# Performance work log

Hardware: AMD Instinct MI355X
Metric: run time of the kernel (lower is better)

## Reference

```python
import jax, jax.numpy as jnp
import numpy as np

B = 1; NUM_Q = 200; PREFIX = 5; GH = 40; GW = 40; P = GH * GW
N = NUM_Q + PREFIX + P  # 1805, token layout [queries][prefix][patches]
D = 1024; NH = 16; DH = D // NH; NB = 4; NC = 151
NEG = -1e9  # additive stand-in for the boolean SDPA mask


def _ln(x, g, b):
    m = x.mean(-1, keepdims=True)
    v = ((x - m) ** 2).mean(-1, keepdims=True)
    return (x - m) * jax.lax.rsqrt(v + 1e-6) * g + b


def setup_inputs() -> dict:
    key = jax.random.key(0)
    ks = iter(jax.random.split(key, 16))
    rn = lambda shape, s=0.02: jax.random.normal(next(ks), shape, jnp.float32) * s
    return {
        'x_tokens': jax.random.normal(next(ks), (B, PREFIX + P, D), jnp.float32),
        'q_weight': rn((NUM_Q, D), 1.0),
        'norm_g': jnp.ones((D,)), 'norm_b': jnp.zeros((D,)),
        'class_W': rn((D, NC)), 'class_b': jnp.zeros((NC,)),
        'mask_W1': rn((D, D)), 'mask_b1': jnp.zeros((D,)),
        'mask_W2': rn((D, D)), 'mask_b2': jnp.zeros((D,)),
        'mask_W3': rn((D, D)), 'mask_b3': jnp.zeros((D,)),
        'ln1_g': jnp.ones((NB, D)), 'ln1_b': jnp.zeros((NB, D)),
        'ln2_g': jnp.ones((NB, D)), 'ln2_b': jnp.zeros((NB, D)),
        'qkv_W': rn((NB, D, 3 * D)), 'qkv_b': jnp.zeros((NB, 3 * D)),
        'proj_W': rn((NB, D, D)), 'proj_b': jnp.zeros((NB, D)),
        'ls1': 0.1 * jnp.ones((NB, D)), 'ls2': 0.1 * jnp.ones((NB, D)),
        'fc1_W': rn((NB, D, 4 * D)), 'fc1_b': jnp.zeros((NB, 4 * D)),
        'fc2_W': rn((NB, 4 * D, D)), 'fc2_b': jnp.zeros((NB, D)),
    }


def _forward(x_tokens, q_weight, norm_g, norm_b, class_W, class_b,
             mask_W1, mask_b1, mask_W2, mask_b2, mask_W3, mask_b3,
             ln1_g, ln1_b, ln2_g, ln2_b, qkv_W, qkv_b, proj_W, proj_b,
             ls1, ls2, fc1_W, fc1_b, fc2_W, fc2_b):
    scale = 1.0 / np.sqrt(DH)
    gelu = lambda t: jax.nn.gelu(t, approximate=False)  # torch nn.GELU (erf)

    def predict(nx):
        # _predict: class head + 3-layer mask MLP + einsum('bqc,bchw->bqhw') decode
        q = nx[:, :NUM_Q]
        patch = nx[:, NUM_Q + PREFIX:]  # [B, P, D] == patch_tokens_map flattened
        f = gelu(q @ mask_W1 + mask_b1)
        f = gelu(f @ mask_W2 + mask_b2)
        f = f @ mask_W3 + mask_b3
        mask_logits = jnp.einsum('bqc,bpc->bqp', f, patch).reshape(B, NUM_Q, GH, GW)
        class_logits = q @ class_W + class_b
        return mask_logits, class_logits

    def attn_bias(mask_logits):
        # _attn_mask: bilinear interp to grid, >0 threshold, rows=queries, cols=patches.
        # attn_mask_probs == 1 so _disable_attn_mask is a no-op.
        interp = jax.image.resize(mask_logits, (B, NUM_Q, GH, GW), 'bilinear')
        keep = interp.reshape(B, NUM_Q, P) > 0
        qrows = jnp.where(keep, 0.0, NEG)  # [B, q, P]
        return jnp.zeros((B, N, N), jnp.float32).at[:, :NUM_Q, NUM_Q + PREFIX:].set(qrows)

    def block(x, i, bias):
        h = _ln(x, ln1_g[i], ln1_b[i])
        qkv = (h @ qkv_W[i] + qkv_b[i]).reshape(B, N, 3, NH, DH)
        qh = qkv[:, :, 0].transpose(0, 2, 1, 3)  # [B, H, N, DH]
        kh = qkv[:, :, 1].transpose(0, 2, 1, 3)
        vh = qkv[:, :, 2].transpose(0, 2, 1, 3)
        scores = jnp.einsum('bhnd,bhmd->bhnm', qh, kh) * scale + bias[:, None]
        a = jax.nn.softmax(scores, axis=-1)
        o = jnp.einsum('bhnm,bhmd->bhnd', a, vh).transpose(0, 2, 1, 3).reshape(B, N, D)
        x = x + ls1[i] * (o @ proj_W[i] + proj_b[i])
        h2 = _ln(x, ln2_g[i], ln2_b[i])
        x = x + ls2[i] * (gelu(h2 @ fc1_W[i] + fc1_b[i]) @ fc2_W[i] + fc2_b[i])
        return x

    x = jnp.concatenate([jnp.broadcast_to(q_weight, (B, NUM_Q, D)), x_tokens], axis=1)
    masks, classes = [], []
    for i in range(NB):  # fixed 4 late blocks
        nx = _ln(x, norm_g, norm_b)
        m, c = predict(nx)
        masks.append(m); classes.append(c)
        x = block(x, i, attn_bias(m))
    nx = _ln(x, norm_g, norm_b)
    m, c = predict(nx)
    masks.append(m); classes.append(c)
    return jnp.stack(masks), jnp.stack(classes)


def reference(x_tokens, q_weight, norm_g, norm_b, class_W, class_b,
              mask_W1, mask_b1, mask_W2, mask_b2, mask_W3, mask_b3,
              ln1_g, ln1_b, ln2_g, ln2_b, qkv_W, qkv_b, proj_W, proj_b,
              ls1, ls2, fc1_W, fc1_b, fc2_W, fc2_b):
    return _forward(x_tokens, q_weight, norm_g, norm_b, class_W, class_b,
                    mask_W1, mask_b1, mask_W2, mask_b2, mask_W3, mask_b3,
                    ln1_g, ln1_b, ln2_g, ln2_b, qkv_W, qkv_b, proj_W, proj_b,
                    ls1, ls2, fc1_W, fc1_b, fc2_W, fc2_b)
```

## Files before the change

kernel.cpp:

```cpp
#include <hip/hip_runtime.h>
#include <hip/hip_bf16.h>

#define NQ 200
#define PFX 5
#define NPATCH 1600
#define NT 1805
#define DM 1024
#define NHEAD 16
#define DHEAD 64
#define NBLK 4
#define NCLS 151
#define NKT 29
#define NWRD 57

typedef short s16x8 __attribute__((ext_vector_type(8)));
typedef float f32x4 __attribute__((ext_vector_type(4)));

__device__ __forceinline__ float gelu_f(float x) {
  return 0.5f * x * (1.0f + erff(x * 0.7071067811865476f));
}
__device__ __forceinline__ short f2bf(float x) {
  __hip_bfloat16 h = __float2bfloat16(x);
  return *reinterpret_cast<short*>(&h);
}
__device__ __forceinline__ float bf2f(short s) {
  __hip_bfloat16 h;
  *reinterpret_cast<short*>(&h) = s;
  return __bfloat162float(h);
}
__device__ __forceinline__ void glds16(const void* g, void* l) {
  __builtin_amdgcn_global_load_lds(
      (const __attribute__((address_space(1))) void*)g,
      (__attribute__((address_space(3))) void*)l, 16, 0, 0);
}

__global__ __launch_bounds__(256) void concat_kernel(const float* __restrict__ qw,
    const float* __restrict__ xt, float* __restrict__ x) {
  int idx = blockIdx.x * 256 + threadIdx.x;
  if (idx >= NT * DM) return;
  int n = idx >> 10;
  x[idx] = (n < NQ) ? qw[idx] : xt[idx - NQ * DM];
}

__global__ __launch_bounds__(256) void cvtT_kernel(const float* __restrict__ W,
    short* __restrict__ Th, short* __restrict__ Tl, int K, int N) {
  __shared__ float t[32][33];
  const int n0 = blockIdx.x * 32, k0 = blockIdx.y * 32;
  const int tx = threadIdx.x & 31, ty = threadIdx.x >> 5;
#pragma unroll
  for (int i = 0; i < 32; i += 8)
    t[ty + i][tx] = W[(size_t)(k0 + ty + i) * N + n0 + tx];
  __syncthreads();
#pragma unroll
  for (int i = 0; i < 32; i += 8) {
    int n = n0 + ty + i, k = k0 + tx;
    float xv = t[tx][ty + i];
    short hh = f2bf(xv);
    Th[(size_t)n * K + k] = hh;
    Tl[(size_t)n * K + k] = f2bf(xv - bf2f(hh));
  }
}

__global__ __launch_bounds__(256) void ln_kernel(const float* __restrict__ in,
    const float* __restrict__ g, const float* __restrict__ b,
    short* __restrict__ oh, short* __restrict__ ol) {
  const int row = blockIdx.x;
  const int tid = threadIdx.x;
  const float* x = in + (size_t)row * DM;
  float v[4];
#pragma unroll
  for (int i = 0; i < 4; ++i) v[i] = x[tid + (i << 8)];
  float s = v[0] + v[1] + v[2] + v[3];
  __shared__ float red[4];
  __shared__ float red2[4];
#pragma unroll
  for (int off = 32; off; off >>= 1) s += __shfl_down(s, off, 64);
  if ((tid & 63) == 0) red[tid >> 6] = s;
  __syncthreads();
  float mean = (red[0] + red[1] + red[2] + red[3]) * (1.0f / DM);
  float sq = 0.f;
#pragma unroll
  for (int i = 0; i < 4; ++i) { float d = v[i] - mean; sq += d * d; }
#pragma unroll
  for (int off = 32; off; off >>= 1) sq += __shfl_down(sq, off, 64);
  if ((tid & 63) == 0) red2[tid >> 6] = sq;
  __syncthreads();
  float var = (red2[0] + red2[1] + red2[2] + red2[3]) * (1.0f / DM);
  float inv = 1.0f / sqrtf(var + 1e-6f);
#pragma unroll
  for (int i = 0; i < 4; ++i) {
    int d = tid + (i << 8);
    float y = (v[i] - mean) * inv * g[d] + b[d];
    short hh = f2bf(y);
    oh[(size_t)row * DM + d] = hh;
    ol[(size_t)row * DM + d] = f2bf(y - bf2f(hh));
  }
}

template <int BM64, int BSRC, int ALO, int ACT, int OMODE, int KS>
__global__ __launch_bounds__(256) void mgemm_kernel(
    const short* __restrict__ Ah, const short* __restrict__ Al,
    const float* __restrict__ Wf,
    const short* __restrict__ Bh, const short* __restrict__ Bl,
    const float* __restrict__ bias, const float* __restrict__ lsv,
    float* __restrict__ Cf, short* __restrict__ Ch, short* __restrict__ Cl,
    int M, int N, int K) {
  constexpr int BM = BM64 ? 64 : 128;
  constexpr int AT = BM64 ? 2 : 4;
  constexpr int AISS = BM64 ? 1 : 2;
  __shared__ __align__(16) short sAh[2 * BM * 32];
  __shared__ __align__(16) short sAl[ALO ? 2 * BM * 32 : 8];
  __shared__ __align__(16) short sBh[2 * 128 * 32], sBl[2 * 128 * 32];
  const int tid = threadIdx.x;
  const int lane = tid & 63;
  const int w = tid >> 6;
  const int bm = blockIdx.y * BM;
  const int bn = blockIdx.x << 7;
  const int z = (KS > 1) ? blockIdx.z : 0;
  const int KL = K / KS;
  const int kbase = z * KL;

  f32x4 acc[AT][4];
  {
    f32x4 zf = {0.f, 0.f, 0.f, 0.f};
#pragma unroll
    for (int mi = 0; mi < AT; ++mi)
#pragma unroll
      for (int ni = 0; ni < 4; ++ni) acc[mi][ni] = zf;
  }

  auto issueA = [&](int buf, int k0) {
#pragma unroll
    for (int i = 0; i < AISS; ++i) {
      int br = (BM64 ? (w << 4) : (w << 5) + (i << 4));
      int r = br + (lane >> 2);
      int cg = (lane & 3) ^ ((r >> 1) & 3);
      size_t go = (size_t)min(bm + r, M - 1) * K + kbase + k0 + (cg << 3);
      glds16(Ah + go, &sAh[(buf * BM + br) * 32]);
      if (ALO) glds16(Al + go, &sAl[(buf * BM + br) * 32]);
    }
  };
  auto issueB1 = [&](int buf, int k0) {
#pragma unroll
    for (int i = 0; i < 2; ++i) {
      int br = (w << 5) + (i << 4);
      int r = br + (lane >> 2);
      int cg = (lane & 3) ^ ((r >> 1) & 3);
      size_t go = (size_t)min(bn + r, N - 1) * K + kbase + k0 + (cg << 3);
      glds16(Bh + go, &sBh[(buf * 128 + br) * 32]);
      glds16(Bl + go, &sBl[(buf * 128 + br) * 32]);
    }
  };
  float wv[2][8];
  auto loadB0 = [&](int k0) {
#pragma unroll
    for (int p = 0; p < 2; ++p) {
      int n = tid & 127;
      int c8 = (tid >> 7) + (p << 1);
      const float* Wp = Wf + (size_t)(kbase + k0 + (c8 << 3)) * N + min(bn + n, N - 1);
#pragma unroll
      for (int j = 0; j < 8; ++j) wv[p][j] = Wp[(size_t)j * N];
    }
  };
  auto writeB0 = [&](int buf) {
#pragma unroll
    for (int p = 0; p < 2; ++p) {
      int n = tid & 127;
      int c8 = (tid >> 7) + (p << 1);
      int cp = c8 ^ ((n >> 1) & 3);
      union { uint4 u; short e[8]; } H, L;
#pragma unroll
      for (int j = 0; j < 8; ++j) {
        short hh = f2bf(wv[p][j]);
        H.e[j] = hh;
        L.e[j] = f2bf(wv[p][j] - bf2f(hh));
      }
      int off = (buf * 128 + n) * 32 + (cp << 3);
      *(uint4*)&sBh[off] = H.u;
      *(uint4*)&sBl[off] = L.u;
    }
  };

  issueA(0, 0);
  if (BSRC == 1) issueB1(0, 0);
  else { loadB0(0); writeB0(0); }
  __syncthreads();

  const int nt = KL >> 5;
  int cur = 0;
  const int ar = lane & 15;
  const int kc = lane >> 4;
  const int wmr = BM64 ? ((w >> 1) << 5) : ((w >> 1) << 6);
  const int wnr = (w & 1) << 6;

  for (int t = 0; t < nt; ++t) {
    const bool more = (t + 1 < nt);
    if (more) {
      int k0n = (t + 1) << 5;
      issueA(cur ^ 1, k0n);
      if (BSRC == 1) issueB1(cur ^ 1, k0n);
      else loadB0(k0n);
    }
    s16x8 fah[AT], fal[AT], fbh[4], fbl[4];
#pragma unroll
    for (int t2 = 0; t2 < AT; ++t2) {
      int r = wmr + (t2 << 4) + ar;
      int off = (cur * BM + r) * 32 + ((kc ^ ((r >> 1) & 3)) << 3);
      fah[t2] = *(const s16x8*)&sAh[off];
      if (ALO) fal[t2] = *(const s16x8*)&sAl[off];
    }
#pragma unroll
    for (int t2 = 0; t2 < 4; ++t2) {
      int r = wnr + (t2 << 4) + ar;
      int off = (cur * 128 + r) * 32 + ((kc ^ ((r >> 1) & 3)) << 3);
      fbh[t2] = *(const s16x8*)&sBh[off];
      fbl[t2] = *(const s16x8*)&sBl[off];
    }
#pragma unroll
    for (int mi = 0; mi < AT; ++mi)
#pragma unroll
      for (int ni = 0; ni < 4; ++ni) {
        acc[mi][ni] = __builtin_amdgcn_mfma_f32_16x16x32_bf16(fah[mi], fbh[ni], acc[mi][ni], 0, 0, 0);
        acc[mi][ni] = __builtin_amdgcn_mfma_f32_16x16x32_bf16(fah[mi], fbl[ni], acc[mi][ni], 0, 0, 0);
        if (ALO)
          acc[mi][ni] = __builtin_amdgcn_mfma_f32_16x16x32_bf16(fal[mi], fbh[ni], acc[mi][ni], 0, 0, 0);
      }
    if (more) {
      if (BSRC == 0) writeB0(cur ^ 1);
      __syncthreads();
      cur ^= 1;
    }
  }

  const int erow = bm + wmr + ((lane >> 4) << 2);
  const int ecol = bn + wnr + (lane & 15);
  float bv[4], lv[4];
#pragma unroll
  for (int ni = 0; ni < 4; ++ni) {
    int col = ecol + ni * 16;
    float b0 = (bias != nullptr && col < N) ? bias[col] : 0.f;
    bv[ni] = (KS > 1 && z != 0) ? 0.f : b0;
    lv[ni] = (OMODE == 5 && col < N) ? lsv[col] : 0.f;
  }
#pragma unroll
  for (int mi = 0; mi < AT; ++mi) {
#pragma unroll
    for (int rr = 0; rr < 4; ++rr) {
      int row = erow + mi * 16 + rr;
      if (row >= M) continue;
#pragma unroll
      for (int ni = 0; ni < 4; ++ni) {
        int col = ecol + ni * 16;
        if (col >= N) continue;
        float v = acc[mi][ni][rr] + bv[ni];
        size_t o = (size_t)row * N + col;
        if (OMODE == 0) {
          if (ACT == 1) v = gelu_f(v);
          short hh = f2bf(v);
          Ch[o] = hh;
          Cl[o] = f2bf(v - bf2f(hh));
        } else if (OMODE == 1) {
          if (ACT == 1) v = gelu_f(v);
          Cf[o] = v;
        } else if (OMODE == 2) {
          atomicAdd(&Cf[o], v);
        } else if (OMODE == 3) {
          Cf[(size_t)z * M * N + o] = v;
        } else if (OMODE == 4) {
          if (ACT == 1) v = gelu_f(v);
          Ch[o] = f2bf(v);
        } else if (OMODE == 5) {
          atomicAdd(&Cf[o], lv[ni] * v);
        } else {
          short hh = f2bf(v);
          Ch[o] = hh;
          if (col < 1024) Cl[o] = f2bf(v - bf2f(hh));
        }
      }
    }
  }
}

template <int ACT, int WSPLIT>
__global__ __launch_bounds__(256) void redsplit_kernel(const float* __restrict__ pb,
    float* __restrict__ outf, short* __restrict__ oh, short* __restrict__ ol,
    int KSr, int MN) {
  int idx = blockIdx.x * 256 + threadIdx.x;
  if (idx >= MN) return;
  float s = 0.f;
  for (int zz = 0; zz < KSr; ++zz) s += pb[(size_t)zz * MN + idx];
  if (ACT == 1) s = gelu_f(s);
  if (WSPLIT) {
    short hh = f2bf(s);
    oh[idx] = hh;
    ol[idx] = f2bf(s - bf2f(hh));
  } else {
    outf[idx] = s;
  }
}

__global__ __launch_bounds__(256) void maskpack_kernel(const float* __restrict__ mlog,
    unsigned* __restrict__ bits) {
  int idx = blockIdx.x * 256 + threadIdx.x;
  if (idx >= NQ * NWRD) return;
  int q = idx / NWRD, w = idx - q * NWRD;
  unsigned word = 0u;
  int c0 = w * 32;
#pragma unroll
  for (int b = 0; b < 32; ++b) {
    int c = c0 + b;
    unsigned keep;
    if (c < NQ + PFX) keep = 1u;
    else if (c < NT) keep = (mlog[(size_t)q * NPATCH + (c - NQ - PFX)] > 0.f) ? 1u : 0u;
    else keep = 0u;
    word |= keep << b;
  }
  bits[idx] = word;
}

__global__ __launch_bounds__(256, 2) void fattn_kernel(
    const short* __restrict__ qh, const short* __restrict__ ql,
    const unsigned* __restrict__ bits, short* __restrict__ ao_h) {
  const int bid = blockIdx.x;
  const int h = bid & 15;
  const int q0 = (bid >> 4) * 64;
  const int tid = threadIdx.x;
  const int lane = tid & 63;
  const int w = tid >> 6;
  const int lg = lane >> 4;
  const int lc = lane & 15;

  __shared__ __align__(16) short Kh[2 * 64 * 64];
  __shared__ __align__(16) short Vt[2 * 64 * 64];
  __shared__ __align__(16) short Pp[4][16 * 64];
  __shared__ float fb[4][16];

  s16x8 qfh[2], qfl[2];
  {
    int gq = min(q0 + (w << 4) + lc, NT - 1);
    const size_t base = (size_t)gq * 3072 + h * 64;
#pragma unroll
    for (int ks = 0; ks < 2; ++ks) {
      qfh[ks] = *(const s16x8*)(qh + base + ks * 32 + (lg << 3));
      qfl[ks] = *(const s16x8*)(ql + base + ks * 32 + (lg << 3));
    }
  }

  const int krow = tid >> 3, kchk = tid & 7;
  const int vrow = tid >> 2, vchk = tid & 3;
  uint4 pkh[2], pvh[2];
  auto loadKV = [&](int kt) {
#pragma unroll
    for (int ii = 0; ii < 2; ++ii) {
      int gk = kt * 64 + krow + (ii << 5);
      if (gk < NT) {
        pkh[ii] = *(const uint4*)(qh + (size_t)gk * 3072 + 1024 + h * 64 + (kchk << 3));
      } else {
        pkh[ii] = make_uint4(0, 0, 0, 0);
      }
      int gv = kt * 64 + vrow;
      int vc = vchk + (ii << 2);
      if (gv < NT) {
        pvh[ii] = *(const uint4*)(qh + (size_t)gv * 3072 + 2048 + h * 64 + (vc << 3));
      } else {
        pvh[ii] = make_uint4(0, 0, 0, 0);
      }
    }
  };
  auto writeKV = [&](int buf) {
    const int bo = buf << 12;
#pragma unroll
    for (int ii = 0; ii < 2; ++ii) {
      int row = krow + (ii << 5);
      *(uint4*)&Kh[bo + (row << 6) + ((kchk ^ (row & 7)) << 3)] = pkh[ii];
      int vc = vchk + (ii << 2);
      const short* vs = (const short*)&pvh[ii];
#pragma unroll
      for (int jj = 0; jj < 8; ++jj) {
        int d = (vc << 3) + jj;
        Vt[bo + (d << 6) + (((vrow >> 3) ^ (d & 7)) << 3) + (vrow & 7)] = vs[jj];
      }
    }
  };

  float rm_r[4], rl_r[4];
#pragma unroll
  for (int r = 0; r < 4; ++r) { rm_r[r] = -3.0e38f; rl_r[r] = 0.f; }
  f32x4 o_acc[4];
  {
    f32x4 zf = {0.f, 0.f, 0.f, 0.f};
#pragma unroll
    for (int nd = 0; nd < 4; ++nd) o_acc[nd] = zf;
  }

  loadKV(0);
  writeKV(0);
  __syncthreads();
  loadKV(1);

  for (int kt = 0; kt < NKT; ++kt) {
    const int cb = (kt & 1) << 12;

    f32x4 sc[4];
    {
      f32x4 zf = {0.f, 0.f, 0.f, 0.f};
#pragma unroll
      for (int ni = 0; ni < 4; ++ni) sc[ni] = zf;
    }
    __builtin_amdgcn_s_setprio(1);
#pragma unroll
    for (int ni = 0; ni < 4; ++ni) {
#pragma unroll
      for (int ks = 0; ks < 2; ++ks) {
        int row = (ni << 4) + lc;
        int ch = ((ks << 2) + lg) ^ (row & 7);
        s16x8 kh = *(const s16x8*)&Kh[cb + (row << 6) + (ch << 3)];
        sc[ni] = __builtin_amdgcn_mfma_f32_16x16x32_bf16(qfh[ks], kh, sc[ni], 0, 0, 0);
        sc[ni] = __builtin_amdgcn_mfma_f32_16x16x32_bf16(qfl[ks], kh, sc[ni], 0, 0, 0);
      }
    }
    __builtin_amdgcn_s_setprio(0);

    unsigned wr0[4], wr1[4];
#pragma unroll
    for (int r = 0; r < 4; ++r) {
      int gq = q0 + (w << 4) + (lg << 2) + r;
      wr0[r] = 0xFFFFFFFFu; wr1[r] = 0xFFFFFFFFu;
      if (gq < NQ) {
        wr0[r] = bits[gq * NWRD + (kt << 1)];
        wr1[r] = ((kt << 1) + 1 < NWRD) ? bits[gq * NWRD + (kt << 1) + 1] : 0u;
      }
    }
    const int kvb = kt << 6;
#pragma unroll
    for (int ni = 0; ni < 4; ++ni) {
      int kv = kvb + (ni << 4) + lc;
      unsigned bitpos = ((ni & 1) << 4) + lc;
#pragma unroll
      for (int r = 0; r < 4; ++r) {
        float sv = sc[ni][r] * 0.125f;
        unsigned wd = (ni < 2) ? wr0[r] : wr1[r];
        if (!((wd >> bitpos) & 1u)) sv -= 1e9f;
        sc[ni][r] = (kv < NT) ? sv : -3.0e38f;
      }
    }

    float fr[4];
#pragma unroll
    for (int r = 0; r < 4; ++r) {
      float tm = fmaxf(fmaxf(sc[0][r], sc[1][r]), fmaxf(sc[2][r], sc[3][r]));
#pragma unroll
      for (int m2 = 1; m2 < 16; m2 <<= 1) tm = fmaxf(tm, __shfl_xor(tm, m2, 64));
      float mnew = fmaxf(rm_r[r], tm);
      float f = __expf(rm_r[r] - mnew);
      float ps = 0.f;
#pragma unroll
      for (int ni = 0; ni < 4; ++ni) {
        float e = __expf(sc[ni][r] - mnew);
        sc[ni][r] = e;
        ps += e;
      }
#pragma unroll
      for (int m2 = 1; m2 < 16; m2 <<= 1) ps += __shfl_xor(ps, m2, 64);
      rm_r[r] = mnew;
      rl_r[r] = rl_r[r] * f + ps;
      fr[r] = f;
    }

    short* P = Pp[w];
#pragma unroll
    for (int ni = 0; ni < 4; ++ni) {
#pragma unroll
      for (int r = 0; r < 4; ++r) {
        int qq = (lg << 2) + r;
        int col = (ni << 4) + lc;
        P[(qq << 6) + (((col >> 3) ^ (qq & 7)) << 3) + (col & 7)] = f2bf(sc[ni][r]);
      }
    }
    if (lc == 0) {
#pragma unroll
      for (int r = 0; r < 4; ++r) fb[w][(lg << 2) + r] = fr[r];
    }
    float fq = fb[w][lc];
#pragma unroll
    for (int nd = 0; nd < 4; ++nd)
#pragma unroll
      for (int r = 0; r < 4; ++r) o_acc[nd][r] *= fq;

    s16x8 pfrag[2];
#pragma unroll
    for (int ks = 0; ks < 2; ++ks)
      pfrag[ks] = *(const s16x8*)&P[(lc << 6) + ((((ks << 2) + lg) ^ (lc & 7)) << 3)];
    __builtin_amdgcn_s_setprio(1);
#pragma unroll
    for (int nd = 0; nd < 4; ++nd) {
      int row = (nd << 4) + lc;
#pragma unroll
      for (int ks = 0; ks < 2; ++ks) {
        s16x8 vh = *(const s16x8*)&Vt[cb + (row << 6) + ((((ks << 2) + lg) ^ (lc & 7)) << 3)];
        o_acc[nd] = __builtin_amdgcn_mfma_f32_16x16x32_bf16(vh, pfrag[ks], o_acc[nd], 0, 0, 0);
      }
    }
    __builtin_amdgcn_s_setprio(0);

    if (kt + 1 < NKT) {
      writeKV((kt + 1) & 1);
      if (kt + 2 < NKT) loadKV(kt + 2);
      __syncthreads();
    }
  }

  if (lc == 0) {
#pragma unroll
    for (int r = 0; r < 4; ++r) fb[w][(lg << 2) + r] = rl_r[r];
  }
  float inv = 1.0f / fb[w][lc];
  int gq = q0 + (w << 4) + lc;
  if (gq < NT) {
#pragma unroll
    for (int nd = 0; nd < 4; ++nd) {
      short hh[4];
#pragma unroll
      for (int r = 0; r < 4; ++r) hh[r] = f2bf(o_acc[nd][r] * inv);
      size_t o = (size_t)gq * DM + h * 64 + (nd << 4) + (lg << 2);
      *(short4*)(ao_h + o) = make_short4(hh[0], hh[1], hh[2], hh[3]);
    }
  }
}

extern "C" void kernel_launch(void* const* d_in, const int* in_sizes, int n_in,
                              void* d_out, int out_size, void* d_ws, size_t ws_size,
                              hipStream_t stream) {
  const float* x_tokens = (const float*)d_in[0];
  const float* q_weight = (const float*)d_in[1];
  const float* norm_g   = (const float*)d_in[2];
  const float* norm_b   = (const float*)d_in[3];
  const float* class_W  = (const float*)d_in[4];
  const float* class_b  = (const float*)d_in[5];
  const float* mask_W1  = (const float*)d_in[6];
  const float* mask_b1  = (const float*)d_in[7];
  const float* mask_W2  = (const float*)d_in[8];
  const float* mask_b2  = (const float*)d_in[9];
  const float* mask_W3  = (const float*)d_in[10];
  const float* mask_b3  = (const float*)d_in[11];
  const float* ln1_g    = (const float*)d_in[12];
  const float* ln1_b    = (const float*)d_in[13];
  const float* ln2_g    = (const float*)d_in[14];
  const float* ln2_b    = (const float*)d_in[15];
  const float* qkv_W    = (const float*)d_in[16];
  const float* qkv_b    = (const float*)d_in[17];
  const float* proj_W   = (const float*)d_in[18];
  const float* proj_b   = (const float*)d_in[19];
  const float* ls1      = (const float*)d_in[20];
  const float* ls2      = (const float*)d_in[21];
  const float* fc1_W    = (const float*)d_in[22];
  const float* fc1_b    = (const float*)d_in[23];
  const float* fc2_W    = (const float*)d_in[24];
  const float* fc2_b    = (const float*)d_in[25];

  float* out = (float*)d_out;

  char* p = (char*)d_ws;
  auto alloc = [&](size_t bytes) {
    char* r = p;
    p += (bytes + 255) & ~(size_t)255;
    return r;
  };
  float* x     = (float*)alloc((size_t)NT * DM * 4);
  short* lnb_h = (short*)alloc((size_t)NT * DM * 2);
  short* lnb_l = (short*)alloc((size_t)NT * DM * 2);
  char*  A1    = alloc((size_t)NT * 4 * DM * 4);
  char*  A2    = alloc((size_t)NT * 4 * DM * 2);
  unsigned* bias_bits = (unsigned*)alloc((size_t)NQ * NWRD * 4);

  short* qkvh  = (short*)A1;
  short* qkvl  = qkvh + (size_t)NT * 3 * DM;
  short* fTh   = (short*)A1;
  short* fTl   = fTh + (size_t)4 * DM * DM;
  short* f1_h = (short*)A1;
  short* f1_l = f1_h + (size_t)NQ * DM;
  short* f2_h = f1_l + (size_t)NQ * DM;
  short* f2_l = f2_h + (size_t)NQ * DM;
  short* f3_h = f2_l + (size_t)NQ * DM;
  short* f3_l = f3_h + (size_t)NQ * DM;
  float* pbuf = (float*)(A1 + ((size_t)4 << 20));
  short* qTh   = (short*)A2;
  short* qTl   = qTh + (size_t)3 * DM * DM;
  short* aoh   = (short*)A2;
  short* pTh   = (short*)(A2 + (size_t)NT * DM * 4);
  short* pTl   = pTh + (size_t)DM * DM;
  short* g1h   = (short*)A2;

  const int ELEM_GRID = (NT * DM + 255) / 256;
  auto g128 = [](int M, int Nc, int ks) { return dim3((Nc + 127) / 128, (M + 127) / 128, ks); };
  auto g64  = [](int M, int Nc, int ks) { return dim3((Nc + 127) / 128, (M + 63) / 64, ks); };
  auto rgrid = [](int n) { return dim3((n + 255) / 256); };
  auto cgrid = [](int K, int N) { return dim3(N / 32, K / 32); };

  concat_kernel<<<ELEM_GRID, 256, 0, stream>>>(q_weight, x_tokens, x);

  for (int i = 0; i <= NBLK; ++i) {
    ln_kernel<<<NT, 256, 0, stream>>>(x, norm_g, norm_b, lnb_h, lnb_l);
    float* mask_i = out + (size_t)i * NQ * NPATCH;
    float* cls_i  = out + (size_t)5 * NQ * NPATCH + (size_t)i * NQ * NCLS;
    mgemm_kernel<1, 0, 1, 0, 3, 8><<<g64(NQ, DM, 8), 256, 0, stream>>>(
        lnb_h, lnb_l, mask_W1, nullptr, nullptr, mask_b1, nullptr, pbuf, nullptr, nullptr, NQ, DM, DM);
    redsplit_kernel<1, 1><<<rgrid(NQ * DM), 256, 0, stream>>>(pbuf, nullptr, f1_h, f1_l, 8, NQ * DM);
    mgemm_kernel<1, 0, 1, 0, 3, 8><<<g64(NQ, DM, 8), 256, 0, stream>>>(
        f1_h, f1_l, mask_W2, nullptr, nullptr, mask_b2, nullptr, pbuf, nullptr, nullptr, NQ, DM, DM);
    redsplit_kernel<1, 1><<<rgrid(NQ * DM), 256, 0, stream>>>(pbuf, nullptr, f2_h, f2_l, 8, NQ * DM);
    mgemm_kernel<1, 0, 1, 0, 3, 8><<<g64(NQ, DM, 8), 256, 0, stream>>>(
        f2_h, f2_l, mask_W3, nullptr, nullptr, mask_b3, nullptr, pbuf, nullptr, nullptr, NQ, DM, DM);
    redsplit_kernel<0, 1><<<rgrid(NQ * DM), 256, 0, stream>>>(pbuf, nullptr, f3_h, f3_l, 8, NQ * DM);
    mgemm_kernel<1, 1, 1, 0, 3, 4><<<g64(NQ, NPATCH, 4), 256, 0, stream>>>(
        f3_h, f3_l, nullptr, lnb_h + (size_t)(NQ + PFX) * DM, lnb_l + (size_t)(NQ + PFX) * DM,
        nullptr, nullptr, pbuf, nullptr, nullptr, NQ, NPATCH, DM);
    redsplit_kernel<0, 0><<<rgrid(NQ * NPATCH), 256, 0, stream>>>(
        pbuf, mask_i, nullptr, nullptr, 4, NQ * NPATCH);
    mgemm_kernel<1, 0, 1, 0, 3, 8><<<g64(NQ, NCLS, 8), 256, 0, stream>>>(
        lnb_h, lnb_l, class_W, nullptr, nullptr, class_b, nullptr, pbuf, nullptr, nullptr, NQ, NCLS, DM);
    redsplit_kernel<0, 0><<<rgrid(NQ * NCLS), 256, 0, stream>>>(
        pbuf, cls_i, nullptr, nullptr, 8, NQ * NCLS);
    if (i == NBLK) break;

    ln_kernel<<<NT, 256, 0, stream>>>(x, ln1_g + i * DM, ln1_b + i * DM, lnb_h, lnb_l);
    cvtT_kernel<<<cgrid(DM, 3 * DM), 256, 0, stream>>>(
        qkv_W + (size_t)i * DM * 3 * DM, qTh, qTl, DM, 3 * DM);
    mgemm_kernel<0, 1, 0, 0, 6, 1><<<g128(NT, 3 * DM, 1), 256, 0, stream>>>(
        lnb_h, lnb_l, nullptr, qTh, qTl, qkv_b + i * 3 * DM, nullptr,
        nullptr, qkvh, qkvl, NT, 3 * DM, DM);
    maskpack_kernel<<<(NQ * NWRD + 255) / 256, 256, 0, stream>>>(mask_i, bias_bits);
    fattn_kernel<<<NKT * NHEAD, 256, 0, stream>>>(qkvh, qkvl, bias_bits, aoh);
    cvtT_kernel<<<cgrid(DM, DM), 256, 0, stream>>>(
        proj_W + (size_t)i * DM * DM, pTh, pTl, DM, DM);
    mgemm_kernel<1, 1, 0, 0, 5, 4><<<g64(NT, DM, 4), 256, 0, stream>>>(
        aoh, nullptr, nullptr, pTh, pTl, proj_b + i * DM, ls1 + i * DM,
        x, nullptr, nullptr, NT, DM, DM);
    ln_kernel<<<NT, 256, 0, stream>>>(x, ln2_g + i * DM, ln2_b + i * DM, lnb_h, lnb_l);
    cvtT_kernel<<<cgrid(DM, 4 * DM), 256, 0, stream>>>(
        fc1_W + (size_t)i * DM * 4 * DM, fTh, fTl, DM, 4 * DM);
    mgemm_kernel<0, 1, 0, 1, 4, 1><<<g128(NT, 4 * DM, 1), 256, 0, stream>>>(
        lnb_h, lnb_l, nullptr, fTh, fTl, fc1_b + i * 4 * DM, nullptr,
        nullptr, g1h, nullptr, NT, 4 * DM, DM);
    cvtT_kernel<<<cgrid(4 * DM, DM), 256, 0, stream>>>(
        fc2_W + (size_t)i * 4 * DM * DM, fTh, fTl, 4 * DM, DM);
    mgemm_kernel<1, 1, 0, 0, 5, 4><<<g64(NT, DM, 4), 256, 0, stream>>>(
        g1h, nullptr, nullptr, fTh, fTl, fc2_b + i * DM, ls2 + i * DM,
        x, nullptr, nullptr, NT, DM, 4 * DM);
  }
}
```

Baseline: 1.576 ms.

## Write V transposed from QKV GEMM and async-load K/V into LDS

The QKV GEMM epilogue now splits its output into three buffers. Q and K go to a 2048-wide buffer, the low part only for Q, and V is written transposed into a padded buffer. The attention kernel then pulls K and V tiles straight into LDS with global_load_lds, with the swizzle applied in the global addresses. This removes register staging and the scalar per-element transposed LDS stores for V. In exchange, the GEMM epilogue does strided, poorly coalesced scattered stores for V. The padded V columns past the last token are never written, so a garbage or NaN value there could leak into the output.

```diff
diff --git a/kernel.cpp b/kernel.cpp
--- a/kernel.cpp
+++ b/kernel.cpp
@@ -12,6 +12,7 @@
 #define NCLS 151
 #define NKT 29
 #define NWRD 57
+#define VTS 1856
 
 typedef short s16x8 __attribute__((ext_vector_type(8)));
 typedef float f32x4 __attribute__((ext_vector_type(4)));
@@ -273,8 +274,14 @@
           atomicAdd(&Cf[o], lv[ni] * v);
         } else {
           short hh = f2bf(v);
-          Ch[o] = hh;
-          if (col < 1024) Cl[o] = f2bf(v - bf2f(hh));
+          if (col < 1024) {
+            Ch[(size_t)row * 2048 + col] = hh;
+            Cl[(size_t)row * 1024 + col] = f2bf(v - bf2f(hh));
+          } else if (col < 2048) {
+            Ch[(size_t)row * 2048 + col] = hh;
+          } else {
+            ((short*)Cf)[(size_t)(col - 2048) * VTS + row] = hh;
+          }
         }
       }
     }
@@ -319,8 +326,9 @@
 }
 
 __global__ __launch_bounds__(256, 2) void fattn_kernel(
-    const short* __restrict__ qh, const short* __restrict__ ql,
-    const unsigned* __restrict__ bits, short* __restrict__ ao_h) {
+    const short* __restrict__ qkh, const short* __restrict__ ql,
+    const short* __restrict__ vt, const unsigned* __restrict__ bits,
+    short* __restrict__ ao_h) {
   const int bid = blockIdx.x;
   const int h = bid & 15;
   const int q0 = (bid >> 4) * 64;
@@ -331,55 +339,30 @@
   const int lc = lane & 15;
 
   __shared__ __align__(16) short Kh[2 * 64 * 64];
-  __shared__ __align__(16) short Vt[2 * 64 * 64];
+  __shared__ __align__(16) short Vs[2 * 64 * 64];
   __shared__ __align__(16) short Pp[4][16 * 64];
   __shared__ float fb[4][16];
 
   s16x8 qfh[2], qfl[2];
   {
     int gq = min(q0 + (w << 4) + lc, NT - 1);
-    const size_t base = (size_t)gq * 3072 + h * 64;
 #pragma unroll
     for (int ks = 0; ks < 2; ++ks) {
-      qfh[ks] = *(const s16x8*)(qh + base + ks * 32 + (lg << 3));
-      qfl[ks] = *(const s16x8*)(ql + base + ks * 32 + (lg << 3));
-    }
-  }
-
-  const int krow = tid >> 3, kchk = tid & 7;
-  const int vrow = tid >> 2, vchk = tid & 3;
-  uint4 pkh[2], pvh[2];
-  auto loadKV = [&](int kt) {
+      qfh[ks] = *(const s16x8*)(qkh + (size_t)gq * 2048 + h * 64 + ks * 32 + (lg << 3));
+      qfl[ks] = *(const s16x8*)(ql + (size_t)gq * 1024 + h * 64 + ks * 32 + (lg << 3));
+    }
+  }
+
+  auto issueKV = [&](int kt, int buf) {
+    const int bo = buf << 12;
 #pragma unroll
     for (int ii = 0; ii < 2; ++ii) {
-      int gk = kt * 64 + krow + (ii << 5);
-      if (gk < NT) {
-        pkh[ii] = *(const uint4*)(qh + (size_t)gk * 3072 + 1024 + h * 64 + (kchk << 3));
-      } else {
-        pkh[ii] = make_uint4(0, 0, 0, 0);
-      }
-      int gv = kt * 64 + vrow;
-      int vc = vchk + (ii << 2);
-      if (gv < NT) {
-        pvh[ii] = *(const uint4*)(qh + (size_t)gv * 3072 + 2048 + h * 64 + (vc << 3));
-      } else {
-        pvh[ii] = make_uint4(0, 0, 0, 0);
-      }
-    }
-  };
-  auto writeKV = [&](int buf) {
-    const int bo = buf << 12;
-#pragma unroll
-    for (int ii = 0; ii < 2; ++ii) {
-      int row = krow + (ii << 5);
-      *(uint4*)&Kh[bo + (row << 6) + ((kchk ^ (row & 7)) << 3)] = pkh[ii];
-      int vc = vchk + (ii << 2);
-      const short* vs = (const short*)&pvh[ii];
-#pragma unroll
-      for (int jj = 0; jj < 8; ++jj) {
-        int d = (vc << 3) + jj;
-        Vt[bo + (d << 6) + (((vrow >> 3) ^ (d & 7)) << 3) + (vrow & 7)] = vs[jj];
-      }
+      int r8 = (((w << 1) + ii) << 3);
+      int row = r8 + (lane >> 3);
+      int cg = (lane & 7) ^ (row & 7);
+      int gk = min(kt * 64 + row, NT - 1);
+      glds16(qkh + (size_t)gk * 2048 + 1024 + h * 64 + (cg << 3), &Kh[bo + (r8 << 6)]);
+      glds16(vt + (size_t)(h * 64 + row) * VTS + kt * 64 + (cg << 3), &Vs[bo + (r8 << 6)]);
     }
   };
 
@@ -393,10 +376,9 @@
     for (int nd = 0; nd < 4; ++nd) o_acc[nd] = zf;
   }
 
-  loadKV(0);
-  writeKV(0);
+  issueKV(0, 0);
   __syncthreads();
-  loadKV(1);
+  issueKV(1, 1);
 
   for (int kt = 0; kt < NKT; ++kt) {
     const int cb = (kt & 1) << 12;
@@ -497,16 +479,15 @@
       int row = (nd << 4) + lc;
 #pragma unroll
       for (int ks = 0; ks < 2; ++ks) {
-        s16x8 vh = *(const s16x8*)&Vt[cb + (row << 6) + ((((ks << 2) + lg) ^ (lc & 7)) << 3)];
+        s16x8 vh = *(const s16x8*)&Vs[cb + (row << 6) + ((((ks << 2) + lg) ^ (row & 7)) << 3)];
         o_acc[nd] = __builtin_amdgcn_mfma_f32_16x16x32_bf16(vh, pfrag[ks], o_acc[nd], 0, 0, 0);
       }
     }
     __builtin_amdgcn_s_setprio(0);
 
     if (kt + 1 < NKT) {
-      writeKV((kt + 1) & 1);
-      if (kt + 2 < NKT) loadKV(kt + 2);
       __syncthreads();
+      if (kt + 2 < NKT) issueKV(kt + 2, kt & 1);
     }
   }
 
@@ -574,7 +555,8 @@
   unsigned* bias_bits = (unsigned*)alloc((size_t)NQ * NWRD * 4);
 
   short* qkvh  = (short*)A1;
-  short* qkvl  = qkvh + (size_t)NT * 3 * DM;
+  short* qkvl  = qkvh + (size_t)NT * 2048;
+  short* vtb   = qkvl + (size_t)NT * 1024;
   short* fTh   = (short*)A1;
   short* fTl   = fTh + (size_t)4 * DM * DM;
   short* f1_h = (short*)A1;
@@ -626,11 +608,11 @@
     ln_kernel<<<NT, 256, 0, stream>>>(x, ln1_g + i * DM, ln1_b + i * DM, lnb_h, lnb_l);
     cvtT_kernel<<<cgrid(DM, 3 * DM), 256, 0, stream>>>(
         qkv_W + (size_t)i * DM * 3 * DM, qTh, qTl, DM, 3 * DM);
-    mgemm_kernel<0, 1, 0, 0, 6, 1><<<g128(NT, 3 * DM, 1), 256, 0, stream>>>(
+    mgemm_kernel<0, 1, 0, 0, 7, 1><<<g128(NT, 3 * DM, 1), 256, 0, stream>>>(
         lnb_h, lnb_l, nullptr, qTh, qTl, qkv_b + i * 3 * DM, nullptr,
-        nullptr, qkvh, qkvl, NT, 3 * DM, DM);
+        (float*)vtb, qkvh, qkvl, NT, 3 * DM, DM);
     maskpack_kernel<<<(NQ * NWRD + 255) / 256, 256, 0, stream>>>(mask_i, bias_bits);
-    fattn_kernel<<<NKT * NHEAD, 256, 0, stream>>>(qkvh, qkvl, bias_bits, aoh);
+    fattn_kernel<<<NKT * NHEAD, 256, 0, stream>>>(qkvh, qkvl, vtb, bias_bits, aoh);
     cvtT_kernel<<<cgrid(DM, DM), 256, 0, stream>>>(
         proj_W + (size_t)i * DM * DM, pTh, pTl, DM, DM);
     mgemm_kernel<1, 1, 0, 0, 5, 4><<<g64(NT, DM, 4), 256, 0, stream>>>(
```

After: 1.546 ms. About the same (-1.9%).
